# Kernel optimization log

Measured on AMD Instinct MI355X. Metric: run time of the kernel, lower is better.

Reference implementation:

```python
import jax, jax.numpy as jnp
import numpy as np

# ---- config (from Mamba2Config defaults) ----
D_MODEL = 1024
D_STATE = 128
D_CONV = 4
EXPAND = 2
HEADDIM = 64
D_INNER = EXPAND * D_MODEL          # 2048
NHEADS = D_INNER // HEADDIM         # 32
CONV_DIM = D_INNER + 2 * D_STATE    # 2304 (ngroups=1)
D_IN_PROJ = 2 * D_INNER + 2 * D_STATE + NHEADS  # 4384
INTER = ((int(D_MODEL * 8 / 3) + 63) // 64) * 64  # 2752
EPS = 1e-6
BATCH, SEQLEN = 2, 1024


def rmsnorm(x, w):
    return x * jax.lax.rsqrt(jnp.mean(x * x, axis=-1, keepdims=True) + EPS) * w


def setup_inputs() -> dict:
    key = jax.random.key(0)
    ks = jax.random.split(key, 16)
    s = 0.02
    return {
        "hidden_states": jax.random.normal(ks[0], (BATCH, SEQLEN, D_MODEL), jnp.float32),
        "norm_w": jnp.ones((D_MODEL,), jnp.float32),
        "in_proj_w": jax.random.normal(ks[1], (D_IN_PROJ, D_MODEL), jnp.float32) * s,
        "conv_w": jax.random.normal(ks[2], (CONV_DIM, D_CONV), jnp.float32) * 0.2,
        "conv_b": jnp.zeros((CONV_DIM,), jnp.float32),
        "dt_bias": jax.random.normal(ks[3], (NHEADS,), jnp.float32) * 0.5,
        "A_log": jnp.log(jax.random.uniform(ks[4], (NHEADS,), jnp.float32, 1.0, 16.0)),
        "D": jnp.ones((NHEADS,), jnp.float32) + jax.random.normal(ks[5], (NHEADS,), jnp.float32) * 0.05,
        "ssm_norm_w": jnp.ones((D_INNER,), jnp.float32),
        "out_proj_w": jax.random.normal(ks[6], (D_MODEL, D_INNER), jnp.float32) * s,
        "post_norm_w": jnp.ones((D_MODEL,), jnp.float32),
        "gate_w": jax.random.normal(ks[7], (INTER, D_MODEL), jnp.float32) * s,
        "up_w": jax.random.normal(ks[8], (INTER, D_MODEL), jnp.float32) * s,
        "down_w": jax.random.normal(ks[9], (D_MODEL, INTER), jnp.float32) * s,
    }


def _mixer(u, in_proj_w, conv_w, conv_b, dt_bias, A_log, D, ssm_norm_w, out_proj_w):
    b, l, _ = u.shape
    zxbcdt = u @ in_proj_w.T                              # (b,l,4384)
    z = zxbcdt[..., :D_INNER]                             # gate
    xBC = zxbcdt[..., D_INNER:D_INNER + CONV_DIM]
    dt = zxbcdt[..., -NHEADS:]

    # causal depthwise conv1d (kernel D_CONV) + SiLU
    xp = jnp.pad(xBC, ((0, 0), (D_CONV - 1, 0), (0, 0)))
    xBC = sum(xp[:, k:k + l, :] * conv_w[:, k] for k in range(D_CONV)) + conv_b
    xBC = jax.nn.silu(xBC)

    xs = xBC[..., :D_INNER].reshape(b, l, NHEADS, HEADDIM)   # (b,l,h,p)
    Bm = xBC[..., D_INNER:D_INNER + D_STATE]                  # (b,l,n)
    Cm = xBC[..., -D_STATE:]                                  # (b,l,n)

    dt = jax.nn.softplus(dt + dt_bias)                        # (b,l,h)
    A = -jnp.exp(A_log)                                       # (h,)

    def step(h, inp):
        dt_t, x_t, B_t, C_t = inp                             # (b,h),(b,h,p),(b,n),(b,n)
        dA = jnp.exp(dt_t * A)                                # (b,h)
        h = h * dA[..., None, None] + jnp.einsum('bh,bhp,bn->bhpn', dt_t, x_t, B_t)
        y_t = jnp.einsum('bhpn,bn->bhp', h, C_t)
        return h, y_t

    h0 = jnp.zeros((b, NHEADS, HEADDIM, D_STATE), u.dtype)
    xsT = (jnp.moveaxis(dt, 1, 0), jnp.moveaxis(xs, 1, 0),
           jnp.moveaxis(Bm, 1, 0), jnp.moveaxis(Cm, 1, 0))
    _, yT = jax.lax.scan(step, h0, xsT)                       # (l,b,h,p)
    y = jnp.moveaxis(yT, 0, 1) + D[None, None, :, None] * xs  # skip term
    y = y.reshape(b, l, D_INNER)

    # gated RMSNorm (norm_before_gate=False): normalize y*silu(z)
    y = rmsnorm(y * jax.nn.silu(z), ssm_norm_w)
    return y @ out_proj_w.T


def reference(hidden_states, norm_w, in_proj_w, conv_w, conv_b, dt_bias, A_log, D,
              ssm_norm_w, out_proj_w, post_norm_w, gate_w, up_w, down_w):
    res = hidden_states
    h = rmsnorm(hidden_states, norm_w)
    h = _mixer(h, in_proj_w, conv_w, conv_b, dt_bias, A_log, D, ssm_norm_w, out_proj_w)
    x = res + h
    res = x
    h = rmsnorm(x, post_norm_w)
    h = (jax.nn.silu(h @ gate_w.T) * (h @ up_w.T)) @ down_w.T  # SwiGLU MLP
    return res + h
```

## Files before the change

### kernel.cpp

```cpp
#include <hip/hip_runtime.h>
#include <hip/hip_bf16.h>

#define SEQLEN   1024
#define NTOK     2048
#define DMODEL   1024
#define DSTATE   128
#define DINNER   2048
#define NHEADS   32
#define HEADDIM  64
#define CONVDIM  2304
#define DINPROJ  4384
#define INTER    2752
#define Q        64
#define NCHUNK   16

typedef __hip_bfloat16 bf16;
typedef unsigned short ushort_t;
typedef __attribute__((ext_vector_type(8))) short bf16x8;
typedef __attribute__((ext_vector_type(4))) float f32x4;
typedef __attribute__((ext_vector_type(4))) unsigned short u16x4;

__device__ __forceinline__ float bf2f(bf16 x) { return __bfloat162float(x); }
__device__ __forceinline__ float bfu2f(ushort_t u) {
    return __uint_as_float(((unsigned)u) << 16);
}
__device__ __forceinline__ ushort_t f2bfu(float x) {
    union { bf16 h; ushort_t u; } c; c.h = __float2bfloat16(x); return c.u;
}

__device__ __forceinline__ void glds16(const void* g, void* l) {
    __builtin_amdgcn_global_load_lds(
        (const __attribute__((address_space(1))) void*)g,
        (__attribute__((address_space(3))) void*)l, 16, 0, 0);
}

template <int N>
__device__ __forceinline__ void pipe_fence() {
    if constexpr (N == 4)
        asm volatile("s_waitcnt vmcnt(4) lgkmcnt(0)" ::: "memory");
    else if constexpr (N == 2)
        asm volatile("s_waitcnt vmcnt(2) lgkmcnt(0)" ::: "memory");
    else
        asm volatile("s_waitcnt vmcnt(0) lgkmcnt(0)" ::: "memory");
    __builtin_amdgcn_s_barrier();
    __builtin_amdgcn_sched_barrier(0);
}

__device__ inline float block_reduce_sum(float v) {
    __shared__ float red[4];
    #pragma unroll
    for (int off = 32; off >= 1; off >>= 1) v += __shfl_down(v, off);
    int lane = threadIdx.x & 63, w = threadIdx.x >> 6;
    if (lane == 0) red[w] = v;
    __syncthreads();
    return red[0] + red[1] + red[2] + red[3];
}

__global__ __launch_bounds__(256) void f2bf_kernel(
    const float* __restrict__ src, ushort_t* __restrict__ dst, int n)
{
    const int i = (blockIdx.x * 256 + threadIdx.x) * 4;
    if (i < n) {
        const f32x4 v = *(const f32x4*)(src + i);
        u16x4 o;
        #pragma unroll
        for (int k = 0; k < 4; k++) o[k] = f2bfu(v[k]);
        *(u16x4*)(dst + i) = o;
    }
}

#define NWOP (DMODEL * DINNER)
#define NWG  (INTER * DMODEL)
__global__ __launch_bounds__(256) void convert_weights_kernel(
    const float* __restrict__ wop, const float* __restrict__ wg,
    const float* __restrict__ wu, const float* __restrict__ wd,
    ushort_t* __restrict__ dWop, ushort_t* __restrict__ dWgu,
    ushort_t* __restrict__ dWdn)
{
    const int i4 = (blockIdx.x * 256 + threadIdx.x) * 4;
    const float* src;
    ushort_t* dst;
    if (i4 < NWOP) { src = wop + i4; dst = dWop + i4; }
    else if (i4 < NWOP + NWG) {
        const int e = i4 - NWOP, row = e >> 10, col = e & 1023;
        src = wg + e; dst = dWgu + ((size_t)(2 * row) << 10) + col;
    } else if (i4 < NWOP + 2 * NWG) {
        const int e = i4 - NWOP - NWG, row = e >> 10, col = e & 1023;
        src = wu + e; dst = dWgu + ((size_t)(2 * row + 1) << 10) + col;
    } else if (i4 < NWOP + 3 * NWG) {
        const int e = i4 - NWOP - 2 * NWG;
        src = wd + e; dst = dWdn + e;
    } else return;
    const f32x4 v = *(const f32x4*)src;
    u16x4 o;
    #pragma unroll
    for (int k = 0; k < 4; k++) o[k] = f2bfu(v[k]);
    *(u16x4*)dst = o;
}

__global__ __launch_bounds__(256) void rmsnorm1024_kernel(
    const float* __restrict__ x, const float* __restrict__ w, bf16* __restrict__ out)
{
    const int token = blockIdx.x, t = threadIdx.x;
    float v[4]; float ss = 0.f;
    #pragma unroll
    for (int i = 0; i < 4; i++) {
        v[i] = x[(size_t)token * DMODEL + t * 4 + i];
        ss += v[i] * v[i];
    }
    ss = block_reduce_sum(ss);
    const float scale = rsqrtf(ss * (1.0f / DMODEL) + 1e-6f);
    #pragma unroll
    for (int i = 0; i < 4; i++)
        out[(size_t)token * DMODEL + t * 4 + i] =
            __float2bfloat16(v[i] * scale * w[t * 4 + i]);
}

template <int EPI, int MT, int NT>
__global__ __launch_bounds__(256) void gemm_bf(
    const bf16* __restrict__ A, const bf16* __restrict__ W,
    float* __restrict__ Cf, const float* __restrict__ resid_f,
    bf16* __restrict__ out_bf, int M, int N, int K)
{
    __shared__ ushort_t As[3][MT * 32];
    __shared__ ushort_t Bs[3][NT * 32];
    const int tid = threadIdx.x;
    const int w = tid >> 6, lane = tid & 63;
    constexpr int NLD = MT / 64 + NT / 64;

    const int gdx = gridDim.x, gdy = gridDim.y;
    const int nwg = gdx * gdy;
    const int orig = blockIdx.x + gdx * blockIdx.y;
    const int q8 = nwg >> 3, r8 = nwg & 7;
    const int xcd = orig & 7, lin = orig >> 3;
    const int wg = (xcd < r8 ? xcd * (q8 + 1) : r8 * (q8 + 1) + (xcd - r8) * q8) + lin;
    const int m0 = (wg % gdy) * MT;
    const int n0 = (wg / gdy) * NT;

    const int srow = tid >> 2;
    const int scol = (((tid & 3) ^ ((srow >> 1) & 3)) * 8);
    const bf16* Agp[MT / 64];
    const bf16* Wgp[NT / 64];
    #pragma unroll
    for (int i = 0; i < MT / 64; i++)
        Agp[i] = A + (size_t)(m0 + i * 64 + srow) * K + scol;
    #pragma unroll
    for (int i = 0; i < NT / 64; i++) {
        const int nr = n0 + i * 64 + srow;
        Wgp[i] = W + (size_t)(nr < N ? nr : 0) * K + scol;
    }

    const int wy = w >> 1, wx = w & 1;
    const int fr = lane & 15;
    const int fq = lane >> 4;
    const int cxor = (fr >> 1) & 3;
    constexpr int MI = MT / 32;
    constexpr int NJ = NT / 32;
    f32x4 acc[MI][NJ];
    #pragma unroll
    for (int i = 0; i < MI; i++)
        #pragma unroll
        for (int j = 0; j < NJ; j++)
            acc[i][j] = (f32x4){0.f, 0.f, 0.f, 0.f};

    const int nk = K >> 5;

    #define STAGE(buf, koff) do {                                         \
        ushort_t* sa_ = &As[buf][w * 512];                                \
        ushort_t* sb_ = &Bs[buf][w * 512];                                \
        _Pragma("unroll")                                                 \
        for (int i_ = 0; i_ < MT / 64; i_++)                              \
            glds16(Agp[i_] + (koff), sa_ + i_ * 2048);                    \
        _Pragma("unroll")                                                 \
        for (int i_ = 0; i_ < NT / 64; i_++)                              \
            glds16(Wgp[i_] + (koff), sb_ + i_ * 2048);                    \
    } while (0)

    STAGE(0, 0);
    STAGE(1, 32);
    pipe_fence<NLD>();

    int cur = 0, stg = 2;
    for (int kt = 0; kt < nk; ++kt) {
        const bool pf = (kt + 2 < nk);
        if (pf) STAGE(stg, (kt + 2) << 5);
        const ushort_t* ca = As[cur];
        const ushort_t* cb = Bs[cur];
        bf16x8 af[MI], bfv[NJ];
        #pragma unroll
        for (int i = 0; i < MI; i++) {
            const int r = wy * (MT / 2) + i * 16 + fr;
            af[i] = *(const bf16x8*)&ca[r * 32 + ((fq ^ cxor) * 8)];
        }
        #pragma unroll
        for (int j = 0; j < NJ; j++) {
            const int r = wx * (NT / 2) + j * 16 + fr;
            bfv[j] = *(const bf16x8*)&cb[r * 32 + ((fq ^ cxor) * 8)];
        }
        #pragma unroll
        for (int i = 0; i < MI; i++)
            #pragma unroll
            for (int j = 0; j < NJ; j++)
                acc[i][j] = __builtin_amdgcn_mfma_f32_16x16x32_bf16(
                    af[i], bfv[j], acc[i][j], 0, 0, 0);
        if (pf)               pipe_fence<NLD>();
        else if (kt + 1 < nk) pipe_fence<0>();
        cur = (cur == 2) ? 0 : cur + 1;
        stg = (stg == 2) ? 0 : stg + 1;
    }
    #undef STAGE

    #pragma unroll
    for (int i = 0; i < MI; i++) {
        #pragma unroll
        for (int j = 0; j < NJ; j++) {
            const int mb = m0 + wy * (MT / 2) + i * 16 + (lane >> 4) * 4;
            const int nn = n0 + wx * (NT / 2) + j * 16 + (lane & 15);
            if (nn < N) {
                #pragma unroll
                for (int r = 0; r < 4; r++) {
                    if (EPI == 2) {
                        const float g = acc[i][j][r];
                        const float u = __shfl_xor(g, 1);
                        if (!(lane & 1)) {
                            const float a = (g / (1.f + expf(-g))) * u;
                            out_bf[(size_t)(mb + r) * (N / 2) + (nn >> 1)] =
                                __float2bfloat16(a);
                        }
                    } else {
                        const size_t idx = (size_t)(mb + r) * N + nn;
                        float v = acc[i][j][r];
                        if (EPI == 1) v += resid_f[idx];
                        Cf[idx] = v;
                    }
                }
            }
        }
    }
}

__global__ __launch_bounds__(256) void conv_silu_kernel(
    const float* __restrict__ zx, const float* __restrict__ cw,
    const float* __restrict__ cb, ushort_t* __restrict__ out)
{
    const int idx = blockIdx.x * 256 + threadIdx.x;
    if (idx >= NTOK * CONVDIM) return;
    const int c = idx % CONVDIM;
    const int token = idx / CONVDIM;
    const int l = token & (SEQLEN - 1);
    float acc = cb[c];
    #pragma unroll
    for (int k = 0; k < 4; k++) {
        const int ls = l - 3 + k;
        if (ls >= 0)
            acc += zx[(size_t)(token - 3 + k) * DINPROJ + DINNER + c] * cw[c * 4 + k];
    }
    out[(size_t)token * CONVDIM + c] = f2bfu(acc / (1.f + expf(-acc)));
}

__global__ __launch_bounds__(256) void dt_softplus_kernel(
    const float* __restrict__ zx, const float* __restrict__ dtb,
    float* __restrict__ out)
{
    const int idx = blockIdx.x * 256 + threadIdx.x;
    const int h = idx & (NHEADS - 1);
    const int token = idx >> 5;
    float v = zx[(size_t)token * DINPROJ + (DINNER + CONVDIM) + h] + dtb[h];
    out[idx] = (v > 20.f) ? v : log1pf(expf(v));
}

__global__ __launch_bounds__(256) void chunk_state_kernel(
    const ushort_t* __restrict__ cvb, const float* __restrict__ dtb,
    const float* __restrict__ A_log, float* __restrict__ ccum,
    ushort_t* __restrict__ Sbuf)
{
    const int bx = blockIdx.x;
    const int bh = bx >> 4, c = bx & 15;
    const int b = bh >> 5, h = bh & 31;
    const int t = threadIdx.x;
    const int w = t >> 6, lane = t & 63;
    const int wy = w >> 1, wx = w & 1;
    const int fr = lane & 15, fk = (lane >> 4) * 8, cr = (lane >> 4) * 4;
    const int tok0 = b * SEQLEN + c * Q;
    const float A = -expf(A_log[h]);

    __shared__ ushort_t sXT[64 * 88];
    __shared__ ushort_t sBT[128 * 88];
    __shared__ float sW[64];

    if (t < 64) {
        const float d = dtb[(size_t)(tok0 + t) * NHEADS + h];
        float s = d;
        #pragma unroll
        for (int off = 1; off < 64; off <<= 1) {
            const float up = __shfl_up(s, off);
            if (t >= off) s += up;
        }
        const float total = __shfl(s, 63);
        sW[t] = expf(A * (total - s)) * d;
        if (t == 63) ccum[bh * NCHUNK + c] = A * total;
    }
    __syncthreads();

    for (int i = t; i < 64 * 64; i += 256) {
        const int l = i >> 6, p = i & 63;
        const float v = bfu2f(cvb[(size_t)(tok0 + l) * CONVDIM + h * HEADDIM + p]);
        sXT[p * 88 + l] = f2bfu(sW[l] * v);
    }
    for (int i = t; i < 128 * 64; i += 256) {
        const int l = i >> 7, n = i & 127;
        sBT[n * 88 + l] = cvb[(size_t)(tok0 + l) * CONVDIM + DINNER + n];
    }
    __syncthreads();

    f32x4 acc[2][4];
    #pragma unroll
    for (int i = 0; i < 2; i++)
        #pragma unroll
        for (int j = 0; j < 4; j++)
            acc[i][j] = (f32x4){0.f, 0.f, 0.f, 0.f};
    #pragma unroll
    for (int k0 = 0; k0 < 64; k0 += 32) {
        bf16x8 af[2], bfv[4];
        #pragma unroll
        for (int i = 0; i < 2; i++)
            af[i] = *(const bf16x8*)&sXT[(wy * 32 + i * 16 + fr) * 88 + fk + k0];
        #pragma unroll
        for (int j = 0; j < 4; j++)
            bfv[j] = *(const bf16x8*)&sBT[(wx * 64 + j * 16 + fr) * 88 + fk + k0];
        #pragma unroll
        for (int i = 0; i < 2; i++)
            #pragma unroll
            for (int j = 0; j < 4; j++)
                acc[i][j] = __builtin_amdgcn_mfma_f32_16x16x32_bf16(
                    af[i], bfv[j], acc[i][j], 0, 0, 0);
    }
    const size_t slot = (size_t)(bh * NCHUNK + c) * 64 * 128;
    #pragma unroll
    for (int i = 0; i < 2; i++) {
        #pragma unroll
        for (int j = 0; j < 4; j++) {
            #pragma unroll
            for (int r = 0; r < 4; r++) {
                const int pr = wy * 32 + i * 16 + cr + r;
                const int nn = wx * 64 + j * 16 + fr;
                Sbuf[slot + pr * 128 + nn] = f2bfu(acc[i][j][r]);
            }
        }
    }
}

__global__ __launch_bounds__(256) void stitch_kernel(
    const float* __restrict__ ccum, ushort_t* __restrict__ Sbuf)
{
    const int bh = blockIdx.x >> 2, ng = blockIdx.x & 3;
    const int t = threadIdx.x, p = t >> 2, q = t & 3;
    float H[8];
    #pragma unroll
    for (int j = 0; j < 8; j++) H[j] = 0.f;
    for (int c = 0; c < NCHUNK; c++) {
        const float P = expf(ccum[bh * NCHUNK + c]);
        const size_t slot = ((size_t)(bh * NCHUNK + c) * 64 + p) * 128 + ng * 32;
        #pragma unroll
        for (int jj = 0; jj < 2; jj++) {
            const u16x4 sv4 = *(const u16x4*)&Sbuf[slot + q * 4 + 16 * jj];
            u16x4 hv4;
            #pragma unroll
            for (int k = 0; k < 4; k++) hv4[k] = f2bfu(H[jj * 4 + k]);
            *(u16x4*)&Sbuf[slot + q * 4 + 16 * jj] = hv4;
            #pragma unroll
            for (int k = 0; k < 4; k++)
                H[jj * 4 + k] = P * H[jj * 4 + k] + bfu2f(sv4[k]);
        }
    }
}

__global__ __launch_bounds__(256) void chunk_scan_mfma_kernel(
    const ushort_t* __restrict__ cvb, const float* __restrict__ dtb,
    const float* __restrict__ A_log, const float* __restrict__ Dh,
    const ushort_t* __restrict__ Sbuf, bf16* __restrict__ ybuf)
{
    const int bx = blockIdx.x;
    const int bh = bx >> 4, c = bx & 15;
    const int b = bh >> 5, h = bh & 31;
    const int t = threadIdx.x;
    const int w = t >> 6, lane = t & 63;
    const int wy = w >> 1, wx = w & 1;
    const int fr = lane & 15;
    const int fk = (lane >> 4) * 8;
    const int cr = (lane >> 4) * 4;
    const int tok0 = b * SEQLEN + c * Q;
    const float A = -expf(A_log[h]);
    const float Dv = Dh[h];

    __shared__ ushort_t sB[64 * 136];
    __shared__ ushort_t sC[64 * 136];
    __shared__ ushort_t sH[64 * 136];
    __shared__ ushort_t sXT[64 * 72];
    __shared__ ushort_t sM[64 * 72];
    __shared__ float    sCum[64];
    __shared__ float    sDtv[64];

    for (int i = t; i < 64 * 32; i += 256) {
        const int row = i >> 5, col = (i & 31) * 4;
        const size_t base = (size_t)(tok0 + row) * CONVDIM;
        *(u16x4*)&sB[row * 136 + col] = *(const u16x4*)&cvb[base + DINNER + col];
        *(u16x4*)&sC[row * 136 + col] = *(const u16x4*)&cvb[base + DINNER + DSTATE + col];
    }
    for (int i = t; i < 64 * 32; i += 256) {
        const int p = i >> 5, l0 = (i & 31) * 2;
        const ushort_t x0 = cvb[(size_t)(tok0 + l0)     * CONVDIM + h * HEADDIM + p];
        const ushort_t x1 = cvb[(size_t)(tok0 + l0 + 1) * CONVDIM + h * HEADDIM + p];
        *(unsigned*)&sXT[p * 72 + l0] = ((unsigned)x1 << 16) | x0;
    }
    {
        const size_t slot = (size_t)(bh * NCHUNK + c) * 64 * 128;
        for (int i = t * 4; i < 64 * 128; i += 1024) {
            const int row = i >> 7, col = i & 127;
            *(u16x4*)&sH[row * 136 + col] = *(const u16x4*)&Sbuf[slot + row * 128 + col];
        }
    }
    if (t < 64) {
        const float d = dtb[(size_t)(tok0 + t) * NHEADS + h];
        float s = d;
        #pragma unroll
        for (int off = 1; off < 64; off <<= 1) {
            const float up = __shfl_up(s, off);
            if (t >= off) s += up;
        }
        sCum[t] = A * s;
        sDtv[t] = d;
    }
    __syncthreads();

    f32x4 accg[2][2];
    #pragma unroll
    for (int i = 0; i < 2; i++)
        #pragma unroll
        for (int j = 0; j < 2; j++)
            accg[i][j] = (f32x4){0.f, 0.f, 0.f, 0.f};
    #pragma unroll
    for (int k0 = 0; k0 < 128; k0 += 32) {
        bf16x8 af[2], bfv[2];
        #pragma unroll
        for (int i = 0; i < 2; i++)
            af[i] = *(const bf16x8*)&sC[(wy * 32 + i * 16 + fr) * 136 + fk + k0];
        #pragma unroll
        for (int j = 0; j < 2; j++)
            bfv[j] = *(const bf16x8*)&sB[(wx * 32 + j * 16 + fr) * 136 + fk + k0];
        #pragma unroll
        for (int i = 0; i < 2; i++)
            #pragma unroll
            for (int j = 0; j < 2; j++)
                accg[i][j] = __builtin_amdgcn_mfma_f32_16x16x32_bf16(
                    af[i], bfv[j], accg[i][j], 0, 0, 0);
    }
    __syncthreads();

    #pragma unroll
    for (int i = 0; i < 2; i++) {
        #pragma unroll
        for (int j = 0; j < 2; j++) {
            #pragma unroll
            for (int r = 0; r < 4; r++) {
                const int l  = wy * 32 + i * 16 + cr + r;
                const int jc = wx * 32 + j * 16 + fr;
                const float v = (jc <= l)
                    ? accg[i][j][r] * expf(sCum[l] - sCum[jc]) * sDtv[jc] : 0.f;
                sM[l * 72 + jc] = f2bfu(v);
            }
        }
    }
    for (int i = t; i < 64 * 32; i += 256) {
        const int row = i >> 5, col = (i & 31) * 4;
        const float sc = expf(sCum[row]);
        u16x4 v = *(const u16x4*)&sC[row * 136 + col];
        #pragma unroll
        for (int k = 0; k < 4; k++) v[k] = f2bfu(bfu2f(v[k]) * sc);
        *(u16x4*)&sC[row * 136 + col] = v;
    }
    __syncthreads();

    f32x4 accy[2][2];
    #pragma unroll
    for (int i = 0; i < 2; i++)
        #pragma unroll
        for (int j = 0; j < 2; j++)
            accy[i][j] = (f32x4){0.f, 0.f, 0.f, 0.f};
    #pragma unroll
    for (int k0 = 0; k0 < 64; k0 += 32) {
        bf16x8 af[2], bfv[2];
        #pragma unroll
        for (int i = 0; i < 2; i++)
            af[i] = *(const bf16x8*)&sM[(wy * 32 + i * 16 + fr) * 72 + fk + k0];
        #pragma unroll
        for (int j = 0; j < 2; j++)
            bfv[j] = *(const bf16x8*)&sXT[(wx * 32 + j * 16 + fr) * 72 + fk + k0];
        #pragma unroll
        for (int i = 0; i < 2; i++)
            #pragma unroll
            for (int j = 0; j < 2; j++)
                accy[i][j] = __builtin_amdgcn_mfma_f32_16x16x32_bf16(
                    af[i], bfv[j], accy[i][j], 0, 0, 0);
    }
    #pragma unroll
    for (int k0 = 0; k0 < 128; k0 += 32) {
        bf16x8 af[2], bfv[2];
        #pragma unroll
        for (int i = 0; i < 2; i++)
            af[i] = *(const bf16x8*)&sC[(wy * 32 + i * 16 + fr) * 136 + fk + k0];
        #pragma unroll
        for (int j = 0; j < 2; j++)
            bfv[j] = *(const bf16x8*)&sH[(wx * 32 + j * 16 + fr) * 136 + fk + k0];
        #pragma unroll
        for (int i = 0; i < 2; i++)
            #pragma unroll
            for (int j = 0; j < 2; j++)
                accy[i][j] = __builtin_amdgcn_mfma_f32_16x16x32_bf16(
                    af[i], bfv[j], accy[i][j], 0, 0, 0);
    }

    #pragma unroll
    for (int i = 0; i < 2; i++) {
        #pragma unroll
        for (int j = 0; j < 2; j++) {
            #pragma unroll
            for (int r = 0; r < 4; r++) {
                const int l = wy * 32 + i * 16 + cr + r;
                const int p = wx * 32 + j * 16 + fr;
                const float x = bfu2f(sXT[p * 72 + l]);
                ybuf[(size_t)(tok0 + l) * DINNER + h * HEADDIM + p] =
                    __float2bfloat16(accy[i][j][r] + Dv * x);
            }
        }
    }
}

__global__ __launch_bounds__(256) void gated_rmsnorm_kernel(
    const bf16* __restrict__ y, const float* __restrict__ zx,
    const float* __restrict__ w, bf16* __restrict__ out)
{
    const int token = blockIdx.x, t = threadIdx.x;
    const bf16* yr = y + (size_t)token * DINNER;
    const float* zr = zx + (size_t)token * DINPROJ;
    float v[8]; float ss = 0.f;
    #pragma unroll
    for (int i = 0; i < 8; i++) {
        const int idx = t * 8 + i;
        const float zz = zr[idx];
        const float val = bf2f(yr[idx]) * (zz / (1.f + expf(-zz)));
        v[i] = val; ss += val * val;
    }
    ss = block_reduce_sum(ss);
    const float scale = rsqrtf(ss * (1.0f / DINNER) + 1e-6f);
    #pragma unroll
    for (int i = 0; i < 8; i++) {
        const int idx = t * 8 + i;
        out[(size_t)token * DINNER + idx] =
            __float2bfloat16(v[i] * scale * w[idx]);
    }
}

extern "C" void kernel_launch(void* const* d_in, const int* in_sizes, int n_in,
                              void* d_out, int out_size, void* d_ws, size_t ws_size,
                              hipStream_t stream) {
    const float* hidden     = (const float*)d_in[0];
    const float* norm_w     = (const float*)d_in[1];
    const float* in_proj_w  = (const float*)d_in[2];
    const float* conv_w     = (const float*)d_in[3];
    const float* conv_b     = (const float*)d_in[4];
    const float* dt_bias    = (const float*)d_in[5];
    const float* A_log      = (const float*)d_in[6];
    const float* Dh         = (const float*)d_in[7];
    const float* ssm_norm_w = (const float*)d_in[8];
    const float* out_proj_w = (const float*)d_in[9];
    const float* post_norm_w= (const float*)d_in[10];
    const float* gate_w     = (const float*)d_in[11];
    const float* up_w       = (const float*)d_in[12];
    const float* down_w     = (const float*)d_in[13];
    float* out = (float*)d_out;

    float* ws = (float*)d_ws;
    bf16*  h_norm = (bf16*)(ws);
    float* zx     = ws + 1048576;
    ushort_t* cvb = (ushort_t*)(ws + 10027008);
    float* dtb    = ws + 14745600;
    float* ccum   = ws + 14811136;
    ushort_t* Sbuf= (ushort_t*)(ws + 14812160);
    float* xbuf   = ws + 19006464;
    bf16*  ybuf   = (bf16*)(ws + 21103616);
    bf16*  ynorm  = (bf16*)(ws + 22152192);
    ushort_t* Wip = (ushort_t*)(ws + 10027008);
    ushort_t* Wop = (ushort_t*)(ws + 1048576);
    ushort_t* Wgu = (ushort_t*)(ws + 2097152);
    ushort_t* Wdn = (ushort_t*)(ws + 4915200);
    bf16*  act    = (bf16*)(ws + 6324224);
    bf16*  h2     = h_norm;

    f2bf_kernel<<<4384, 256, 0, stream>>>(in_proj_w, Wip, DINPROJ * DMODEL);
    rmsnorm1024_kernel<<<NTOK, 256, 0, stream>>>(hidden, norm_w, h_norm);
    gemm_bf<0, 128, 128><<<dim3(35, 16), 256, 0, stream>>>(h_norm, (const bf16*)Wip, zx,
        nullptr, nullptr, NTOK, DINPROJ, DMODEL);
    conv_silu_kernel<<<(NTOK * CONVDIM) / 256, 256, 0, stream>>>(zx, conv_w, conv_b, cvb);
    dt_softplus_kernel<<<(NTOK * NHEADS) / 256, 256, 0, stream>>>(zx, dt_bias, dtb);
    chunk_state_kernel<<<1024, 256, 0, stream>>>(cvb, dtb, A_log, ccum, Sbuf);
    stitch_kernel<<<256, 256, 0, stream>>>(ccum, Sbuf);
    chunk_scan_mfma_kernel<<<1024, 256, 0, stream>>>(cvb, dtb, A_log, Dh, Sbuf, ybuf);
    gated_rmsnorm_kernel<<<NTOK, 256, 0, stream>>>(ybuf, zx, ssm_norm_w, ynorm);
    convert_weights_kernel<<<(NWOP + 3 * NWG) / 1024, 256, 0, stream>>>(
        out_proj_w, gate_w, up_w, down_w, Wop, Wgu, Wdn);
    gemm_bf<1, 64, 64><<<dim3(16, 32), 256, 0, stream>>>(ynorm, (const bf16*)Wop, xbuf,
        hidden, nullptr, NTOK, DMODEL, DINNER);
    rmsnorm1024_kernel<<<NTOK, 256, 0, stream>>>(xbuf, post_norm_w, h2);
    gemm_bf<2, 128, 128><<<dim3(43, 16), 256, 0, stream>>>(h2, (const bf16*)Wgu,
        nullptr, nullptr, act, NTOK, 2 * INTER, DMODEL);
    gemm_bf<1, 64, 64><<<dim3(16, 32), 256, 0, stream>>>(act, (const bf16*)Wdn, out,
        xbuf, nullptr, NTOK, DMODEL, INTER);
}
```

Measured before the change: 357.7 us.

## Fuse conv-SiLU with dt softplus and add specialized small-tile residual GEMM

Measured after the change: 333.0 us. -6.9%, faster.

```diff
diff --git a/kernel.cpp b/kernel.cpp
--- a/kernel.cpp
+++ b/kernel.cpp
@@ -239,34 +239,154 @@
     }
 }
 
-__global__ __launch_bounds__(256) void conv_silu_kernel(
+__global__ __launch_bounds__(256) void gemm_bf_s(
+    const bf16* __restrict__ A, const bf16* __restrict__ W,
+    float* __restrict__ Cf, const float* __restrict__ resid_f,
+    int M, int N, int K)
+{
+    constexpr int MT = 64, NT = 64;
+    __shared__ ushort_t As[2][MT * 64];
+    __shared__ ushort_t Bs[2][NT * 64];
+    const int tid = threadIdx.x;
+    const int w = tid >> 6, lane = tid & 63;
+
+    const int gdx = gridDim.x, gdy = gridDim.y;
+    const int nwg = gdx * gdy;
+    const int orig = blockIdx.x + gdx * blockIdx.y;
+    const int q8 = nwg >> 3, r8 = nwg & 7;
+    const int xcd = orig & 7, lin = orig >> 3;
+    const int wg = (xcd < r8 ? xcd * (q8 + 1) : r8 * (q8 + 1) + (xcd - r8) * q8) + lin;
+    const int m0 = (wg % gdy) * MT;
+    const int n0 = (wg / gdy) * NT;
+
+    const int srow = tid >> 3;
+    const int scol = (((tid & 7) ^ (srow & 7)) * 8);
+    const bf16* Agp[2];
+    const bf16* Wgp[2];
+    #pragma unroll
+    for (int i = 0; i < 2; i++)
+        Agp[i] = A + (size_t)(m0 + i * 32 + srow) * K + scol;
+    #pragma unroll
+    for (int i = 0; i < 2; i++) {
+        const int nr = n0 + i * 32 + srow;
+        Wgp[i] = W + (size_t)(nr < N ? nr : 0) * K + scol;
+    }
+
+    const int wy = w >> 1, wx = w & 1;
+    const int fr = lane & 15;
+    const int fq = lane >> 4;
+    f32x4 acc[2][2];
+    #pragma unroll
+    for (int i = 0; i < 2; i++)
+        #pragma unroll
+        for (int j = 0; j < 2; j++)
+            acc[i][j] = (f32x4){0.f, 0.f, 0.f, 0.f};
+
+    const int nk = K >> 6;
+
+    #define STAGE_S(buf, koff) do {                                       \
+        ushort_t* sa_ = &As[buf][w * 512];                                \
+        ushort_t* sb_ = &Bs[buf][w * 512];                                \
+        _Pragma("unroll")                                                 \
+        for (int i_ = 0; i_ < 2; i_++)                                    \
+            glds16(Agp[i_] + (koff), sa_ + i_ * 2048);                    \
+        _Pragma("unroll")                                                 \
+        for (int i_ = 0; i_ < 2; i_++)                                    \
+            glds16(Wgp[i_] + (koff), sb_ + i_ * 2048);                    \
+    } while (0)
+
+    STAGE_S(0, 0);
+    __syncthreads();
+
+    for (int kt = 0; kt < nk; ++kt) {
+        const int cur = kt & 1;
+        if (kt + 1 < nk) STAGE_S(cur ^ 1, (kt + 1) << 6);
+        const ushort_t* ca = As[cur];
+        const ushort_t* cb = Bs[cur];
+        #pragma unroll
+        for (int ks = 0; ks < 2; ks++) {
+            bf16x8 af[2], bfv[2];
+            #pragma unroll
+            for (int i = 0; i < 2; i++) {
+                const int r = wy * 32 + i * 16 + fr;
+                const int g = ks * 4 + fq;
+                af[i] = *(const bf16x8*)&ca[r * 64 + ((g ^ (r & 7)) * 8)];
+            }
+            #pragma unroll
+            for (int j = 0; j < 2; j++) {
+                const int r = wx * 32 + j * 16 + fr;
+                const int g = ks * 4 + fq;
+                bfv[j] = *(const bf16x8*)&cb[r * 64 + ((g ^ (r & 7)) * 8)];
+            }
+            #pragma unroll
+            for (int i = 0; i < 2; i++)
+                #pragma unroll
+                for (int j = 0; j < 2; j++)
+                    acc[i][j] = __builtin_amdgcn_mfma_f32_16x16x32_bf16(
+                        af[i], bfv[j], acc[i][j], 0, 0, 0);
+        }
+        __syncthreads();
+    }
+    #undef STAGE_S
+
+    #pragma unroll
+    for (int i = 0; i < 2; i++) {
+        #pragma unroll
+        for (int j = 0; j < 2; j++) {
+            const int mb = m0 + wy * 32 + i * 16 + (lane >> 4) * 4;
+            const int nn = n0 + wx * 32 + j * 16 + (lane & 15);
+            if (nn < N) {
+                #pragma unroll
+                for (int r = 0; r < 4; r++) {
+                    const size_t idx = (size_t)(mb + r) * N + nn;
+                    Cf[idx] = acc[i][j][r] + resid_f[idx];
+                }
+            }
+        }
+    }
+}
+
+#define NCONVBLK ((NTOK * CONVDIM / 4) / 256)
+__global__ __launch_bounds__(256) void conv_silu_dt_kernel(
     const float* __restrict__ zx, const float* __restrict__ cw,
-    const float* __restrict__ cb, ushort_t* __restrict__ out)
-{
-    const int idx = blockIdx.x * 256 + threadIdx.x;
-    if (idx >= NTOK * CONVDIM) return;
-    const int c = idx % CONVDIM;
-    const int token = idx / CONVDIM;
-    const int l = token & (SEQLEN - 1);
-    float acc = cb[c];
-    #pragma unroll
-    for (int k = 0; k < 4; k++) {
-        const int ls = l - 3 + k;
-        if (ls >= 0)
-            acc += zx[(size_t)(token - 3 + k) * DINPROJ + DINNER + c] * cw[c * 4 + k];
-    }
-    out[(size_t)token * CONVDIM + c] = f2bfu(acc / (1.f + expf(-acc)));
-}
-
-__global__ __launch_bounds__(256) void dt_softplus_kernel(
-    const float* __restrict__ zx, const float* __restrict__ dtb,
-    float* __restrict__ out)
-{
-    const int idx = blockIdx.x * 256 + threadIdx.x;
-    const int h = idx & (NHEADS - 1);
-    const int token = idx >> 5;
-    float v = zx[(size_t)token * DINPROJ + (DINNER + CONVDIM) + h] + dtb[h];
-    out[idx] = (v > 20.f) ? v : log1pf(expf(v));
+    const float* __restrict__ cb, const float* __restrict__ dtbias,
+    ushort_t* __restrict__ out, float* __restrict__ dtb_out)
+{
+    const int bid = blockIdx.x;
+    if (bid < NCONVBLK) {
+        const int i = bid * 256 + threadIdx.x;
+        const int cg = i % (CONVDIM / 4);
+        const int token = i / (CONVDIM / 4);
+        const int c0 = cg * 4;
+        const int l = token & (SEQLEN - 1);
+        float a[4];
+        #pragma unroll
+        for (int j = 0; j < 4; j++) a[j] = cb[c0 + j];
+        f32x4 cwv[4];
+        #pragma unroll
+        for (int j = 0; j < 4; j++) cwv[j] = *(const f32x4*)(cw + (c0 + j) * 4);
+        #pragma unroll
+        for (int k = 0; k < 4; k++) {
+            const int ls = l - 3 + k;
+            if (ls >= 0) {
+                const f32x4 v = *(const f32x4*)(
+                    zx + (size_t)(token - 3 + k) * DINPROJ + DINNER + c0);
+                #pragma unroll
+                for (int j = 0; j < 4; j++) a[j] += v[j] * cwv[j][k];
+            }
+        }
+        u16x4 o;
+        #pragma unroll
+        for (int j = 0; j < 4; j++)
+            o[j] = f2bfu(a[j] / (1.f + expf(-a[j])));
+        *(u16x4*)(out + (size_t)token * CONVDIM + c0) = o;
+    } else {
+        const int idx = (bid - NCONVBLK) * 256 + threadIdx.x;
+        const int h = idx & (NHEADS - 1);
+        const int token = idx >> 5;
+        float v = zx[(size_t)token * DINPROJ + (DINNER + CONVDIM) + h] + dtbias[h];
+        dtb_out[idx] = (v > 20.f) ? v : log1pf(expf(v));
+    }
 }
 
 __global__ __launch_bounds__(256) void chunk_state_kernel(
@@ -601,19 +721,19 @@
     rmsnorm1024_kernel<<<NTOK, 256, 0, stream>>>(hidden, norm_w, h_norm);
     gemm_bf<0, 128, 128><<<dim3(35, 16), 256, 0, stream>>>(h_norm, (const bf16*)Wip, zx,
         nullptr, nullptr, NTOK, DINPROJ, DMODEL);
-    conv_silu_kernel<<<(NTOK * CONVDIM) / 256, 256, 0, stream>>>(zx, conv_w, conv_b, cvb);
-    dt_softplus_kernel<<<(NTOK * NHEADS) / 256, 256, 0, stream>>>(zx, dt_bias, dtb);
+    conv_silu_dt_kernel<<<NCONVBLK + (NTOK * NHEADS) / 256, 256, 0, stream>>>(
+        zx, conv_w, conv_b, dt_bias, cvb, dtb);
     chunk_state_kernel<<<1024, 256, 0, stream>>>(cvb, dtb, A_log, ccum, Sbuf);
     stitch_kernel<<<256, 256, 0, stream>>>(ccum, Sbuf);
     chunk_scan_mfma_kernel<<<1024, 256, 0, stream>>>(cvb, dtb, A_log, Dh, Sbuf, ybuf);
     gated_rmsnorm_kernel<<<NTOK, 256, 0, stream>>>(ybuf, zx, ssm_norm_w, ynorm);
     convert_weights_kernel<<<(NWOP + 3 * NWG) / 1024, 256, 0, stream>>>(
         out_proj_w, gate_w, up_w, down_w, Wop, Wgu, Wdn);
-    gemm_bf<1, 64, 64><<<dim3(16, 32), 256, 0, stream>>>(ynorm, (const bf16*)Wop, xbuf,
-        hidden, nullptr, NTOK, DMODEL, DINNER);
+    gemm_bf_s<<<dim3(16, 32), 256, 0, stream>>>(ynorm, (const bf16*)Wop, xbuf,
+        hidden, NTOK, DMODEL, DINNER);
     rmsnorm1024_kernel<<<NTOK, 256, 0, stream>>>(xbuf, post_norm_w, h2);
     gemm_bf<2, 128, 128><<<dim3(43, 16), 256, 0, stream>>>(h2, (const bf16*)Wgu,
         nullptr, nullptr, act, NTOK, 2 * INTER, DMODEL);
-    gemm_bf<1, 64, 64><<<dim3(16, 32), 256, 0, stream>>>(act, (const bf16*)Wdn, out,
-        xbuf, nullptr, NTOK, DMODEL, INTER);
-}
+    gemm_bf_s<<<dim3(16, 32), 256, 0, stream>>>(act, (const bf16*)Wdn, out,
+        xbuf, NTOK, DMODEL, INTER);
+}
```
